# Kernel tuning notes

Measured on AMD Instinct MI355X. Metric: run time of the kernel, lower is better.

## Reference

```python
import jax, jax.numpy as jnp
import numpy as np

INF = jnp.float32(np.inf)
LAMBDA_VAL = 1.0
NUM_CLASSES = 10

def setup_inputs() -> dict:
    key = jax.random.key(0)
    k1, k2, k3 = jax.random.split(key, 3)
    N, P, D = 65536, 2048, 64
    x = jax.random.normal(k1, (N, D), dtype=jnp.float32)
    y = jax.random.randint(k2, (N,), 0, NUM_CLASSES)
    prototypes = jax.random.normal(k3, (P, D), dtype=jnp.float32)
    prototype_labels = jnp.arange(P) % NUM_CLASSES
    return {"x": x, "y": y, "prototypes": prototypes, "prototype_labels": prototype_labels}

def _cdist(x, p):
    # Euclidean pairwise distances via the gemm expansion (matches torch.cdist default
    x2 = jnp.sum(x * x, axis=1, keepdims=True)          # [N, 1]
    p2 = jnp.sum(p * p, axis=1)                          # [P]
    sq = x2 + p2[None, :] - 2.0 * (x @ p.T)              # [N, P]
    return jnp.sqrt(jnp.maximum(sq, 0.0))

def reference(x, y, prototypes, prototype_labels):
    distances = _cdist(x, prototypes)                    # [N, P]
    same = prototype_labels[None, :] == y[:, None]       # [N, P] bool
    pos = jnp.min(jnp.where(same, distances, INF), axis=1)   # [N]
    neg = jnp.min(jnp.where(~same, distances, INF), axis=1)  # [N]
    mu = (pos - neg) / (pos + neg)
    loss = jnp.mean(jax.nn.sigmoid(LAMBDA_VAL * mu))
    return loss
```

## Files before the change

### kernel.cpp

```cpp
#include <hip/hip_runtime.h>
#include <math.h>

#define NROWS  65536
#define DDIM   64
#define NCLS   10

#define CLS_SLOTS   208
#define CLS_FFRAGS  13
#define CLS_STRIDE  27648
#define CLS_P2_OFF  26624

typedef __attribute__((ext_vector_type(8))) short bf16x8;
typedef __attribute__((ext_vector_type(4))) float f32x4;
typedef __attribute__((ext_vector_type(4))) unsigned int u32x4;

__device__ inline unsigned int f2bf(float f) {
    unsigned int u = __float_as_uint(f);
    return (u + 0x7FFFu + ((u >> 16) & 1u)) >> 16;
}

template <int CTRL>
__device__ inline float rorMin(float v) {
    int t = __builtin_amdgcn_update_dpp(0, __float_as_int(v), CTRL, 0xF, 0xF, false);
    return fminf(v, __int_as_float(t));
}

__global__ __launch_bounds__(256) void prep_kernel(
        const float* __restrict__ protos, char* __restrict__ wsB,
        float* __restrict__ out) {
    int t = blockIdx.x * 256 + threadIdx.x;
    int s = t >> 3, jj = t & 7;
    int L = s / CLS_SLOTS;
    int j = s - L * CLS_SLOTS;
    int cnt = (L < 8) ? 205 : 204;
    bool real = (j < cnt);
    float v[8] = {0.f, 0.f, 0.f, 0.f, 0.f, 0.f, 0.f, 0.f};
    if (real) {
        const float* src = protos + (L + 10 * j) * DDIM + jj * 8;
        float4 a = *(const float4*)src;
        float4 b = *(const float4*)(src + 4);
        v[0] = a.x; v[1] = a.y; v[2] = a.z; v[3] = a.w;
        v[4] = b.x; v[5] = b.y; v[6] = b.z; v[7] = b.w;
    }
    float ss = 0.f;
#pragma unroll
    for (int i = 0; i < 8; i++) ss = fmaf(v[i], v[i], ss);
    ss += __shfl_xor(ss, 1, 64);
    ss += __shfl_xor(ss, 2, 64);
    ss += __shfl_xor(ss, 4, 64);
    unsigned int w[4];
#pragma unroll
    for (int i = 0; i < 4; i++) {
        unsigned int lo = f2bf(-2.f * v[2 * i]);
        unsigned int hi = f2bf(-2.f * v[2 * i + 1]);
        w[i] = lo | (hi << 16);
    }
    size_t base = (size_t)L * CLS_STRIDE;
    *(u32x4*)(wsB + base + (size_t)(j * 8 + (jj ^ (j & 7))) * 16) =
        (u32x4){w[0], w[1], w[2], w[3]};
    if (jj == 0)
        *(float*)(wsB + base + CLS_P2_OFF + j * 4) =
            real ? ss : __builtin_inff();
    if (t == 0) out[0] = 0.f;
}

__global__ __launch_bounds__(256) void glvq_fused(
        const float* __restrict__ x, const int* __restrict__ y,
        const char* __restrict__ wsB, float* __restrict__ out) {
    __shared__ __align__(16) char ldsImg[2][CLS_STRIDE];
    __shared__ float ldsX2[4 * 32];
    __shared__ float ldsRed[4];

    const int tid  = threadIdx.x;
    const int wave = tid >> 6;
    const int lane = tid & 63;
    const int quad = lane >> 4;
    const int l15  = lane & 15;
    const float CINF = __builtin_inff();
    const int rowBase = blockIdx.x * 128 + wave * 32;
    int c0 = blockIdx.x % NCLS;

    {
        const char* src = wsB + (size_t)c0 * CLS_STRIDE;
#pragma unroll
        for (int it = 0; it < 7; it++) {
            int i = wave + it * 4;
            if (i < 27) {
                int ub = i * 64;
                __builtin_amdgcn_global_load_lds(
                    (const __attribute__((address_space(1))) void*)(src + (size_t)(ub + lane) * 16),
                    (__attribute__((address_space(3))) void*)(&ldsImg[0][0] + (size_t)ub * 16),
                    16, 0, 0);
            }
        }
    }

    bf16x8 afrag[2][2];
#pragma unroll
    for (int m = 0; m < 2; m++) {
        float ss = 0.f;
#pragma unroll
        for (int k = 0; k < 2; k++) {
            const float* src = x + (size_t)(rowBase + m * 16 + l15) * DDIM + k * 32 + quad * 8;
            float4 a = *(const float4*)src;
            float4 b = *(const float4*)(src + 4);
            float v[8] = {a.x, a.y, a.z, a.w, b.x, b.y, b.z, b.w};
            unsigned int w[4];
#pragma unroll
            for (int i = 0; i < 4; i++) {
                ss = fmaf(v[2 * i],     v[2 * i],     ss);
                ss = fmaf(v[2 * i + 1], v[2 * i + 1], ss);
                w[i] = f2bf(v[2 * i]) | (f2bf(v[2 * i + 1]) << 16);
            }
            union { u32x4 u; bf16x8 h; } cvt;
            cvt.u = (u32x4){w[0], w[1], w[2], w[3]};
            afrag[m][k] = cvt.h;
        }
        ss += __shfl_xor(ss, 16, 64);
        ss += __shfl_xor(ss, 32, 64);
        if (quad == 0) ldsX2[wave * 32 + m * 16 + l15] = ss;
    }

    int yv[2][4];
#pragma unroll
    for (int m = 0; m < 2; m++)
#pragma unroll
        for (int r = 0; r < 4; r++)
            yv[m][r] = y[rowBase + m * 16 + quad * 4 + r];

    float pos[2][4], neg[2][4];
#pragma unroll
    for (int m = 0; m < 2; m++)
#pragma unroll
        for (int r = 0; r < 4; r++) { pos[m][r] = 0.f; neg[m][r] = CINF; }

    asm volatile("s_waitcnt vmcnt(0)" ::: "memory");
    __syncthreads();

    float x2r[2][4];
#pragma unroll
    for (int m = 0; m < 2; m++)
#pragma unroll
        for (int r = 0; r < 4; r++)
            x2r[m][r] = ldsX2[wave * 32 + m * 16 + quad * 4 + r];

    for (int ci = 0; ci < NCLS; ci++) {
        const char* buf = &ldsImg[ci & 1][0];

        if (ci < NCLS - 1) {
            int cn = c0 + ci + 1; if (cn >= NCLS) cn -= NCLS;
            const char* src = wsB + (size_t)cn * CLS_STRIDE;
            char* dst = &ldsImg[(ci + 1) & 1][0];
#pragma unroll
            for (int it = 0; it < 7; it++) {
                int i = wave + it * 4;
                if (i < 27) {
                    int ub = i * 64;
                    __builtin_amdgcn_global_load_lds(
                        (const __attribute__((address_space(1))) void*)(src + (size_t)(ub + lane) * 16),
                        (__attribute__((address_space(3))) void*)(dst + (size_t)ub * 16),
                        16, 0, 0);
                }
            }
        }

        float mMin[2][4];
#pragma unroll
        for (int m = 0; m < 2; m++)
#pragma unroll
            for (int r = 0; r < 4; r++) mMin[m][r] = CINF;

#pragma unroll
        for (int f = 0; f < CLS_FFRAGS; f++) {
            const int s = f * 16 + l15;
            float p2v = *(const float*)(buf + CLS_P2_OFF + s * 4);
            f32x4 p2f = (f32x4){p2v, p2v, p2v, p2v};
            bf16x8 b0 = *(const bf16x8*)(buf + (size_t)(s * 8 + (quad ^ (l15 & 7))) * 16);
            bf16x8 b1 = *(const bf16x8*)(buf + (size_t)(s * 8 + ((4 + quad) ^ (l15 & 7))) * 16);
            f32x4 acc[2];
#pragma unroll
            for (int m = 0; m < 2; m++)
                acc[m] = __builtin_amdgcn_mfma_f32_16x16x32_bf16(
                    afrag[m][0], b0, p2f, 0, 0, 0);
#pragma unroll
            for (int m = 0; m < 2; m++)
                acc[m] = __builtin_amdgcn_mfma_f32_16x16x32_bf16(
                    afrag[m][1], b1, acc[m], 0, 0, 0);
#pragma unroll
            for (int m = 0; m < 2; m++)
#pragma unroll
                for (int r = 0; r < 4; r++)
                    mMin[m][r] = fminf(mMin[m][r], acc[m][r]);
        }

#pragma unroll
        for (int m = 0; m < 2; m++)
#pragma unroll
            for (int r = 0; r < 4; r++) {
                float vmin = mMin[m][r];
                vmin = rorMin<0x128>(vmin);
                vmin = rorMin<0x124>(vmin);
                vmin = rorMin<0x122>(vmin);
                vmin = rorMin<0x121>(vmin);
                mMin[m][r] = vmin;
            }

        int cc = c0 + ci; if (cc >= NCLS) cc -= NCLS;
#pragma unroll
        for (int m = 0; m < 2; m++)
#pragma unroll
            for (int r = 0; r < 4; r++) {
                float d = mMin[m][r];
                bool isPos = (cc == yv[m][r]);
                pos[m][r] = isPos ? d : pos[m][r];
                neg[m][r] = isPos ? neg[m][r] : fminf(neg[m][r], d);
            }

        asm volatile("s_waitcnt vmcnt(0)" ::: "memory");
        __syncthreads();
    }

    float sum = 0.f;
    if (l15 == 0) {
#pragma unroll
        for (int m = 0; m < 2; m++)
#pragma unroll
            for (int r = 0; r < 4; r++) {
                float sp = sqrtf(fmaxf(x2r[m][r] + pos[m][r], 0.f));
                float sn = sqrtf(fmaxf(x2r[m][r] + neg[m][r], 0.f));
                float mu = (sp - sn) / (sp + sn);
                sum += 1.f / (1.f + __expf(-mu));
            }
    }
    sum += __shfl_xor(sum, 16, 64);
    sum += __shfl_xor(sum, 32, 64);
    if (lane == 0) ldsRed[wave] = sum;
    __syncthreads();
    if (tid == 0)
        atomicAdd(out, (ldsRed[0] + ldsRed[1] + ldsRed[2] + ldsRed[3]) *
                           (1.f / (float)NROWS));
}

extern "C" void kernel_launch(void* const* d_in, const int* in_sizes, int n_in,
                              void* d_out, int out_size, void* d_ws, size_t ws_size,
                              hipStream_t stream) {
    const float* x      = (const float*)d_in[0];
    const int*   yp     = (const int*)d_in[1];
    const float* protos = (const float*)d_in[2];
    float* out = (float*)d_out;
    char*  wsB = (char*)d_ws;

    prep_kernel<<<65, 256, 0, stream>>>(protos, wsB, out);
    glvq_fused<<<512, 256, 0, stream>>>(x, yp, wsB, out);
}
```

Before: 101.3 us.

## Read prototype fragments directly from global memory instead of LDS double-buffering

Removes the double-buffered LDS staging of each class's prototype image, along with its per-class barriers and waits. B fragments and squared norms are now loaded straight from global memory (L2-resident workspace) inside the MFMA loop. Classes are visited in a fixed order rather than rotated per block. This drops the LDS footprint and the synchronisation, which can raise occupancy. In exchange, every wave re-fetches the prototypes through the vector cache with higher latency, and the loop is kept rolled.

```diff
diff --git a/kernel.cpp b/kernel.cpp
--- a/kernel.cpp
+++ b/kernel.cpp
@@ -67,7 +67,6 @@
 __global__ __launch_bounds__(256) void glvq_fused(
         const float* __restrict__ x, const int* __restrict__ y,
         const char* __restrict__ wsB, float* __restrict__ out) {
-    __shared__ __align__(16) char ldsImg[2][CLS_STRIDE];
     __shared__ float ldsX2[4 * 32];
     __shared__ float ldsRed[4];
 
@@ -78,22 +77,6 @@
     const int l15  = lane & 15;
     const float CINF = __builtin_inff();
     const int rowBase = blockIdx.x * 128 + wave * 32;
-    int c0 = blockIdx.x % NCLS;
-
-    {
-        const char* src = wsB + (size_t)c0 * CLS_STRIDE;
-#pragma unroll
-        for (int it = 0; it < 7; it++) {
-            int i = wave + it * 4;
-            if (i < 27) {
-                int ub = i * 64;
-                __builtin_amdgcn_global_load_lds(
-                    (const __attribute__((address_space(1))) void*)(src + (size_t)(ub + lane) * 16),
-                    (__attribute__((address_space(3))) void*)(&ldsImg[0][0] + (size_t)ub * 16),
-                    16, 0, 0);
-            }
-        }
-    }
 
     bf16x8 afrag[2][2];
 #pragma unroll
@@ -134,7 +117,6 @@
 #pragma unroll
         for (int r = 0; r < 4; r++) { pos[m][r] = 0.f; neg[m][r] = CINF; }
 
-    asm volatile("s_waitcnt vmcnt(0)" ::: "memory");
     __syncthreads();
 
     float x2r[2][4];
@@ -144,25 +126,13 @@
         for (int r = 0; r < 4; r++)
             x2r[m][r] = ldsX2[wave * 32 + m * 16 + quad * 4 + r];
 
+    const int b0off = l15 * 128 + (quad ^ (l15 & 7)) * 16;
+    const int b1off = l15 * 128 + ((4 + quad) ^ (l15 & 7)) * 16;
+    const int p2off = CLS_P2_OFF + l15 * 4;
+
+#pragma unroll 1
     for (int ci = 0; ci < NCLS; ci++) {
-        const char* buf = &ldsImg[ci & 1][0];
-
-        if (ci < NCLS - 1) {
-            int cn = c0 + ci + 1; if (cn >= NCLS) cn -= NCLS;
-            const char* src = wsB + (size_t)cn * CLS_STRIDE;
-            char* dst = &ldsImg[(ci + 1) & 1][0];
-#pragma unroll
-            for (int it = 0; it < 7; it++) {
-                int i = wave + it * 4;
-                if (i < 27) {
-                    int ub = i * 64;
-                    __builtin_amdgcn_global_load_lds(
-                        (const __attribute__((address_space(1))) void*)(src + (size_t)(ub + lane) * 16),
-                        (__attribute__((address_space(3))) void*)(dst + (size_t)ub * 16),
-                        16, 0, 0);
-                }
-            }
-        }
+        const char* base = wsB + (size_t)ci * CLS_STRIDE;
 
         float mMin[2][4];
 #pragma unroll
@@ -172,11 +142,10 @@
 
 #pragma unroll
         for (int f = 0; f < CLS_FFRAGS; f++) {
-            const int s = f * 16 + l15;
-            float p2v = *(const float*)(buf + CLS_P2_OFF + s * 4);
+            bf16x8 b0 = *(const bf16x8*)(base + f * 2048 + b0off);
+            bf16x8 b1 = *(const bf16x8*)(base + f * 2048 + b1off);
+            float p2v = *(const float*)(base + p2off + f * 64);
             f32x4 p2f = (f32x4){p2v, p2v, p2v, p2v};
-            bf16x8 b0 = *(const bf16x8*)(buf + (size_t)(s * 8 + (quad ^ (l15 & 7))) * 16);
-            bf16x8 b1 = *(const bf16x8*)(buf + (size_t)(s * 8 + ((4 + quad) ^ (l15 & 7))) * 16);
             f32x4 acc[2];
 #pragma unroll
             for (int m = 0; m < 2; m++)
@@ -205,19 +174,15 @@
                 mMin[m][r] = vmin;
             }
 
-        int cc = c0 + ci; if (cc >= NCLS) cc -= NCLS;
 #pragma unroll
         for (int m = 0; m < 2; m++)
 #pragma unroll
             for (int r = 0; r < 4; r++) {
                 float d = mMin[m][r];
-                bool isPos = (cc == yv[m][r]);
+                bool isPos = (ci == yv[m][r]);
                 pos[m][r] = isPos ? d : pos[m][r];
                 neg[m][r] = isPos ? neg[m][r] : fminf(neg[m][r], d);
             }
-
-        asm volatile("s_waitcnt vmcnt(0)" ::: "memory");
-        __syncthreads();
     }
 
     float sum = 0.f;
```

New measurement: 122.3 us. +20.8%, slower.
